# Performance work log

Hardware: AMD Instinct MI355X
Metric: run time of the kernel (lower is better)

Reference implementation:

```python
import jax, jax.numpy as jnp
import numpy as np

H = 1024
NH = 16
HD = H // NH  # 64

def setup_inputs() -> dict:
    key = jax.random.key(0)
    ks = jax.random.split(key, 6)
    B, S = 2, 2048
    hidden_states = jax.random.normal(ks[0], (B, S, H), dtype=jnp.float32)
    attention_mask = jnp.ones((B, S), dtype=jnp.int32)
    sc = 1.0 / np.sqrt(H)
    Wq = jax.random.normal(ks[1], (H, H), dtype=jnp.float32) * sc
    Wk = jax.random.normal(ks[2], (H, H), dtype=jnp.float32) * sc
    Wv = jax.random.normal(ks[3], (H, H), dtype=jnp.float32) * sc
    Wo = jax.random.normal(ks[4], (H, H), dtype=jnp.float32) * sc
    return {"hidden_states": hidden_states, "attention_mask": attention_mask,
            "Wq": Wq, "Wk": Wk, "Wv": Wv, "Wo": Wo}

def reference(hidden_states, attention_mask, Wq, Wk, Wv, Wo):
    B, S, _ = hidden_states.shape
    # nn.Linear(bias=False): y = x @ W.T
    q = hidden_states @ Wq.T
    k = hidden_states @ Wk.T
    v = hidden_states @ Wv.T
    # [B, NH, S, HD]
    q = q.reshape(B, S, NH, HD).transpose(0, 2, 1, 3)
    k = k.reshape(B, S, NH, HD).transpose(0, 2, 1, 3)
    v = v.reshape(B, S, NH, HD).transpose(0, 2, 1, 3)
    # ELU+1 feature map
    q = jax.nn.elu(q) + 1.0
    k = jax.nn.elu(k) + 1.0
    # [B, NH, S, S]
    attn = jnp.einsum('bhqd,bhkd->bhqk', q, k)
    mask = attention_mask[:, None, None, :]  # [B,1,1,S]
    attn = jnp.where(mask == 0, -jnp.inf, attn)
    attn = jax.nn.softmax(attn, axis=-1)
    # dropout p=0.0 (eval) -> identity
    out = jnp.einsum('bhqk,bhkd->bhqd', attn, v)
    out = out.transpose(0, 2, 1, 3).reshape(B, S, H)
    return out @ Wo.T
```

## Files before the change

### kernel.cpp

```cpp
#include <hip/hip_runtime.h>

#define H_ 1024
#define NH_ 16
#define HD_ 64
#define B_ 2
#define S_ 2048
#define BS_ 4096

typedef _Float16 half8 __attribute__((ext_vector_type(8)));
typedef _Float16 half4_t __attribute__((ext_vector_type(4)));
typedef float floatx4 __attribute__((ext_vector_type(4)));

#define LOG2E 1.44269504088896f

__device__ __forceinline__ void async_copy16(void* lds, const void* g) {
  __builtin_amdgcn_global_load_lds(
      (const __attribute__((address_space(1))) unsigned int*)g,
      (__attribute__((address_space(3))) unsigned int*)lds, 16, 0, 0);
}

__global__ __launch_bounds__(256) void cvt_all(
    const float* __restrict__ hs, const float* __restrict__ wq,
    const float* __restrict__ wk, const float* __restrict__ wv,
    const float* __restrict__ wo,
    _Float16* __restrict__ hs_h, _Float16* __restrict__ w_h) {
  int i = blockIdx.x * 256 + threadIdx.x;
  int idx = i * 4;
  const float* src; _Float16* dst; int off;
  if (idx < BS_ * H_) {
    src = hs; dst = hs_h; off = idx;
  } else {
    int j = idx - BS_ * H_;
    int w = j >> 20;
    off = j & ((1 << 20) - 1);
    src = (w == 0) ? wq : (w == 1) ? wk : (w == 2) ? wv : wo;
    dst = w_h + (size_t)w * (H_ * H_);
  }
  float4 f = *(const float4*)(src + off);
  half4_t o;
  o.x = (_Float16)f.x; o.y = (_Float16)f.y;
  o.z = (_Float16)f.z; o.w = (_Float16)f.w;
  *(half4_t*)(dst + off) = o;
}

__global__ __launch_bounds__(256) void qkv_gemm(
    const _Float16* __restrict__ A, const _Float16* __restrict__ Wall,
    _Float16* __restrict__ qh, _Float16* __restrict__ kh,
    _Float16* __restrict__ vt) {
  const int z = blockIdx.z;
  const _Float16* W = Wall + (size_t)z * (H_ * H_);
  const int rbase = blockIdx.y * 128;
  const int cbase = blockIdx.x * 128;
  __shared__ _Float16 As[128 * 32];
  __shared__ _Float16 Bs[128 * 32];
  const int tid = threadIdx.x, lane = tid & 63, w = tid >> 6;
  const int quad = lane >> 4, l16 = lane & 15;
  const int wr = (w >> 1) * 64, wc = (w & 1) * 64;

  floatx4 zero = {0.f, 0.f, 0.f, 0.f};
  floatx4 acc[4][4];
#pragma unroll
  for (int i = 0; i < 4; ++i)
#pragma unroll
    for (int j = 0; j < 4; ++j) acc[i][j] = zero;

  const int srow = w * 32 + (lane >> 2);
  const int sseg = (lane & 3) * 8;
  const _Float16* Ag = A + (size_t)(rbase + srow) * H_ + sseg;
  const _Float16* Bg = W + (size_t)(cbase + srow) * H_ + sseg;

  for (int k0 = 0; k0 < H_; k0 += 32) {
    async_copy16(&As[(w * 32) * 32], Ag + k0);
    async_copy16(&As[(w * 32 + 16) * 32], Ag + 16 * H_ + k0);
    async_copy16(&Bs[(w * 32) * 32], Bg + k0);
    async_copy16(&Bs[(w * 32 + 16) * 32], Bg + 16 * H_ + k0);
    __syncthreads();
    half8 af[4], bf[4];
#pragma unroll
    for (int t = 0; t < 4; ++t)
      af[t] = *(half8*)&As[(wr + t * 16 + l16) * 32 + quad * 8];
#pragma unroll
    for (int t = 0; t < 4; ++t)
      bf[t] = *(half8*)&Bs[(wc + t * 16 + l16) * 32 + quad * 8];
#pragma unroll
    for (int i = 0; i < 4; ++i)
#pragma unroll
      for (int j = 0; j < 4; ++j)
        acc[i][j] = __builtin_amdgcn_mfma_f32_16x16x32_f16(af[i], bf[j],
                                                           acc[i][j], 0, 0, 0);
    __syncthreads();
  }
#pragma unroll
  for (int i = 0; i < 4; ++i) {
    int r0 = rbase + wr + i * 16 + quad * 4;
    int b = r0 >> 11, sl0 = r0 & (S_ - 1);
#pragma unroll
    for (int j = 0; j < 4; ++j) {
      int col = cbase + wc + j * 16 + l16;
      int h = col >> 6, d = col & 63;
      if (z == 2) {
        half4_t pk;
#pragma unroll
        for (int r = 0; r < 4; ++r) pk[r] = (_Float16)acc[i][j][r];
        *(half4_t*)&vt[((size_t)(b * NH_ + h) * HD_ + d) * S_ + sl0] = pk;
      } else {
        _Float16* outp = (z == 0) ? qh : kh;
        float scale = (z == 0) ? LOG2E : 1.0f;
#pragma unroll
        for (int r = 0; r < 4; ++r) {
          float x = acc[i][j][r];
          x = ((x > 0.f) ? (x + 1.f) : __expf(x)) * scale;
          outp[((size_t)(b * NH_ + h) * S_ + sl0 + r) * HD_ + d] = (_Float16)x;
        }
      }
    }
  }
}

__global__ __launch_bounds__(256, 2) void flash_attn(
    const _Float16* __restrict__ qh, const _Float16* __restrict__ kh,
    const _Float16* __restrict__ vt, const int* __restrict__ mask,
    _Float16* __restrict__ attn_out) {
  const int bh = blockIdx.y, b = bh >> 4, h = bh & 15;
  const int qbase = blockIdx.x * 128;
  const int tid = threadIdx.x, w = tid >> 6, lane = tid & 63;
  const int quad = lane >> 4, l16 = lane & 15;

  __shared__ _Float16 Kt[2][128 * 64];
  __shared__ _Float16 Vt[2][64 * 128];

  const _Float16* Q = qh + (size_t)bh * (S_ * HD_);
  const _Float16* K = kh + (size_t)bh * (S_ * HD_);
  const _Float16* Vg = vt + (size_t)bh * (HD_ * S_);
  const int* Mb = mask + b * S_;

  half8 qf[2][2];
#pragma unroll
  for (int g = 0; g < 2; ++g) {
    int qr = qbase + w * 32 + g * 16 + l16;
    qf[g][0] = *(const half8*)&Q[qr * 64 + quad * 8];
    qf[g][1] = *(const half8*)&Q[qr * 64 + 32 + quad * 8];
  }

  floatx4 zero = {0.f, 0.f, 0.f, 0.f};
  floatx4 o[2][4];
#pragma unroll
  for (int g = 0; g < 2; ++g)
#pragma unroll
    for (int i = 0; i < 4; ++i) o[g][i] = zero;
  float mi[2] = {-3e38f, -3e38f}, li[2] = {0.f, 0.f};

  const int krow_off = lane >> 3;
  const int kslot = lane & 7;
  const int kchunk = kslot ^ (krow_off & 7);
  const int vrow_off = lane >> 4;
  const int vslot = lane & 15;

  {
#pragma unroll
    for (int u = 0; u < 4; ++u) {
      int kl = w * 32 + u * 8;
      async_copy16(&Kt[0][kl * 64], K + (size_t)(kl + krow_off) * 64 + kchunk * 8);
    }
#pragma unroll
    for (int u = 0; u < 4; ++u) {
      int d0 = w * 16 + u * 4 + vrow_off;
      int c0 = vslot ^ (d0 & 15);
      async_copy16(&Vt[0][(w * 16 + u * 4) * 128], Vg + (size_t)d0 * S_ + c0 * 8);
    }
  }

  for (int kt = 0; kt < S_ / 128; ++kt) {
    const int key0 = kt * 128;
    const int buf = kt & 1;
    __syncthreads();
    if (kt < S_ / 128 - 1) {
      const int key1 = key0 + 128;
#pragma unroll
      for (int u = 0; u < 4; ++u) {
        int kl = w * 32 + u * 8;
        async_copy16(&Kt[buf ^ 1][kl * 64],
                     K + (size_t)(key1 + kl + krow_off) * 64 + kchunk * 8);
      }
#pragma unroll
      for (int u = 0; u < 4; ++u) {
        int d0 = w * 16 + u * 4 + vrow_off;
        int c0 = vslot ^ (d0 & 15);
        async_copy16(&Vt[buf ^ 1][(w * 16 + u * 4) * 128],
                     Vg + (size_t)d0 * S_ + key1 + c0 * 8);
      }
    }
    int m0 = Mb[key0 + lane];
    int m1 = Mb[key0 + 64 + lane];

    const _Float16* Kb = &Kt[buf][0];
    const _Float16* Vb = &Vt[buf][0];

    floatx4 sa[2][8];
#pragma unroll
    for (int g = 0; g < 2; ++g)
#pragma unroll
      for (int ct = 0; ct < 8; ++ct) sa[g][ct] = zero;
    {
      int s0 = quad ^ (l16 & 7);
      int s1 = (4 + quad) ^ (l16 & 7);
#pragma unroll
      for (int ct = 0; ct < 8; ++ct) {
        int key = ct * 16 + l16;
        half8 bf0 = *(half8*)&Kb[key * 64 + s0 * 8];
        half8 bf1 = *(half8*)&Kb[key * 64 + s1 * 8];
        sa[0][ct] = __builtin_amdgcn_mfma_f32_16x16x32_f16(bf0, qf[0][0], sa[0][ct], 0, 0, 0);
        sa[0][ct] = __builtin_amdgcn_mfma_f32_16x16x32_f16(bf1, qf[0][1], sa[0][ct], 0, 0, 0);
        sa[1][ct] = __builtin_amdgcn_mfma_f32_16x16x32_f16(bf0, qf[1][0], sa[1][ct], 0, 0, 0);
        sa[1][ct] = __builtin_amdgcn_mfma_f32_16x16x32_f16(bf1, qf[1][1], sa[1][ct], 0, 0, 0);
      }
    }
    if (__any((m0 == 0) || (m1 == 0))) {
#pragma unroll
      for (int ct = 0; ct < 8; ++ct)
#pragma unroll
        for (int r = 0; r < 4; ++r)
          if (Mb[key0 + ct * 16 + quad * 4 + r] == 0) {
            sa[0][ct][r] = -1e30f;
            sa[1][ct][r] = -1e30f;
          }
    }
#pragma unroll
    for (int g = 0; g < 2; ++g) {
      float mx = sa[g][0][0];
#pragma unroll
      for (int ct = 0; ct < 8; ++ct)
#pragma unroll
        for (int r = 0; r < 4; ++r) mx = fmaxf(mx, sa[g][ct][r]);
      mx = fmaxf(mx, __shfl_xor(mx, 16));
      mx = fmaxf(mx, __shfl_xor(mx, 32));
      float mn = fmaxf(mi[g], mx);
      float alpha = __builtin_amdgcn_exp2f(mi[g] - mn);
      mi[g] = mn;
      float rs = 0.f;
#pragma unroll
      for (int ct = 0; ct < 8; ++ct)
#pragma unroll
        for (int r = 0; r < 4; ++r) {
          float p = __builtin_amdgcn_exp2f(sa[g][ct][r] - mn);
          sa[g][ct][r] = p;
          rs += p;
        }
      rs += __shfl_xor(rs, 16);
      rs += __shfl_xor(rs, 32);
      li[g] = li[g] * alpha + rs;
#pragma unroll
      for (int ct2 = 0; ct2 < 4; ++ct2) {
        o[g][ct2][0] *= alpha; o[g][ct2][1] *= alpha;
        o[g][ct2][2] *= alpha; o[g][ct2][3] *= alpha;
      }
    }
#pragma unroll
    for (int ct = 0; ct < 8; ++ct) {
      half4_t p0, p1;
#pragma unroll
      for (int r = 0; r < 4; ++r) {
        p0[r] = (_Float16)sa[0][ct][r];
        p1[r] = (_Float16)sa[1][ct][r];
      }
      int chunk = (2 * ct + (quad >> 1)) ^ l16;
      int off = chunk * 8 + (quad & 1) * 4;
#pragma unroll
      for (int ct2 = 0; ct2 < 4; ++ct2) {
        int d = ct2 * 16 + l16;
        half4_t vf = *(half4_t*)&Vb[d * 128 + off];
        o[0][ct2] = __builtin_amdgcn_mfma_f32_16x16x16f16(vf, p0, o[0][ct2], 0, 0, 0);
        o[1][ct2] = __builtin_amdgcn_mfma_f32_16x16x16f16(vf, p1, o[1][ct2], 0, 0, 0);
      }
    }
  }
#pragma unroll
  for (int g = 0; g < 2; ++g) {
    float inv = 1.0f / li[g];
    int row = qbase + w * 32 + g * 16 + l16;
#pragma unroll
    for (int ct2 = 0; ct2 < 4; ++ct2) {
      half4_t pk;
#pragma unroll
      for (int r = 0; r < 4; ++r) pk[r] = (_Float16)(o[g][ct2][r] * inv);
      int d = ct2 * 16 + quad * 4;
      *(half4_t*)&attn_out[((size_t)(b * S_ + row)) * H_ + h * HD_ + d] = pk;
    }
  }
}

__global__ __launch_bounds__(256) void out_gemm(
    const _Float16* __restrict__ A, const _Float16* __restrict__ W,
    float* __restrict__ out) {
  const int rbase = blockIdx.y * 128;
  const int cbase = blockIdx.x * 64;
  __shared__ _Float16 As[128 * 32];
  __shared__ _Float16 Bs[64 * 32];
  const int tid = threadIdx.x, lane = tid & 63, w = tid >> 6;
  const int quad = lane >> 4, l16 = lane & 15;

  floatx4 zero = {0.f, 0.f, 0.f, 0.f};
  floatx4 acc[2][4];
#pragma unroll
  for (int i = 0; i < 2; ++i)
#pragma unroll
    for (int j = 0; j < 4; ++j) acc[i][j] = zero;

  const int srowA = w * 32 + (lane >> 2);
  const int srowB = w * 16 + (lane >> 2);
  const int sseg = (lane & 3) * 8;
  const _Float16* Ag = A + (size_t)(rbase + srowA) * H_ + sseg;
  const _Float16* Bg = W + (size_t)(cbase + srowB) * H_ + sseg;

  for (int k0 = 0; k0 < H_; k0 += 32) {
    async_copy16(&As[(w * 32) * 32], Ag + k0);
    async_copy16(&As[(w * 32 + 16) * 32], Ag + 16 * H_ + k0);
    async_copy16(&Bs[(w * 16) * 32], Bg + k0);
    __syncthreads();
    half8 af[2], bf[4];
#pragma unroll
    for (int t = 0; t < 2; ++t)
      af[t] = *(half8*)&As[(w * 32 + t * 16 + l16) * 32 + quad * 8];
#pragma unroll
    for (int t = 0; t < 4; ++t)
      bf[t] = *(half8*)&Bs[(t * 16 + l16) * 32 + quad * 8];
#pragma unroll
    for (int i = 0; i < 2; ++i)
#pragma unroll
      for (int j = 0; j < 4; ++j)
        acc[i][j] = __builtin_amdgcn_mfma_f32_16x16x32_f16(af[i], bf[j],
                                                           acc[i][j], 0, 0, 0);
    __syncthreads();
  }
#pragma unroll
  for (int i = 0; i < 2; ++i) {
    int r0 = rbase + w * 32 + i * 16 + quad * 4;
#pragma unroll
    for (int j = 0; j < 4; ++j) {
      int col = cbase + j * 16 + l16;
#pragma unroll
      for (int r = 0; r < 4; ++r)
        out[(size_t)(r0 + r) * H_ + col] = acc[i][j][r];
    }
  }
}

extern "C" void kernel_launch(void* const* d_in, const int* in_sizes, int n_in,
                              void* d_out, int out_size, void* d_ws,
                              size_t ws_size, hipStream_t stream) {
  const float* hs = (const float*)d_in[0];
  const int* mask = (const int*)d_in[1];
  const float* Wq = (const float*)d_in[2];
  const float* Wk = (const float*)d_in[3];
  const float* Wv = (const float*)d_in[4];
  const float* Wo = (const float*)d_in[5];
  float* out = (float*)d_out;

  _Float16* p = (_Float16*)d_ws;
  _Float16* hs_h = p; p += (size_t)BS_ * H_;
  _Float16* w_h = p;  p += (size_t)4 * H_ * H_;
  _Float16* q_h = p;  p += (size_t)BS_ * H_;
  _Float16* k_h = p;  p += (size_t)BS_ * H_;
  _Float16* v_t = p;  p += (size_t)BS_ * H_;
  _Float16* ao_h = p; p += (size_t)BS_ * H_;

  cvt_all<<<8192, 256, 0, stream>>>(hs, Wq, Wk, Wv, Wo, hs_h, w_h);
  qkv_gemm<<<dim3(8, 32, 3), 256, 0, stream>>>(hs_h, w_h, q_h, k_h, v_t);
  flash_attn<<<dim3(16, 32), 256, 0, stream>>>(q_h, k_h, v_t, mask, ao_h);
  out_gemm<<<dim3(16, 32), 256, 0, stream>>>(ao_h, w_h + (size_t)3 * H_ * H_, out);
}
```

Measured before the change: 193.1 us.

## Use 8 waves of 16 query rows each in flash attention and skip redundant rescale

The attention kernel moves from 256 threads, where each wave handles 32 query rows, to 512 threads, where each wave handles 16 rows. Each wave then holds half the accumulator and score registers, which is meant to raise occupancy and hide latency. The wider block loads the shared K/V tiles cooperatively, with fewer copies per thread. The output rescale is skipped when no row maximum grows, and the max and sum reductions are split into independent chains. In exchange, each K fragment read from LDS is reused by only one query group instead of two, so LDS traffic per MFMA doubles.

```diff
diff --git a/kernel.cpp b/kernel.cpp
--- a/kernel.cpp
+++ b/kernel.cpp
@@ -117,7 +117,7 @@
   }
 }
 
-__global__ __launch_bounds__(256, 2) void flash_attn(
+__global__ __launch_bounds__(512, 4) void flash_attn(
     const _Float16* __restrict__ qh, const _Float16* __restrict__ kh,
     const _Float16* __restrict__ vt, const int* __restrict__ mask,
     _Float16* __restrict__ attn_out) {
@@ -134,21 +134,15 @@
   const _Float16* Vg = vt + (size_t)bh * (HD_ * S_);
   const int* Mb = mask + b * S_;
 
-  half8 qf[2][2];
-#pragma unroll
-  for (int g = 0; g < 2; ++g) {
-    int qr = qbase + w * 32 + g * 16 + l16;
-    qf[g][0] = *(const half8*)&Q[qr * 64 + quad * 8];
-    qf[g][1] = *(const half8*)&Q[qr * 64 + 32 + quad * 8];
-  }
+  const int qr = qbase + w * 16 + l16;
+  half8 qf0 = *(const half8*)&Q[qr * 64 + quad * 8];
+  half8 qf1 = *(const half8*)&Q[qr * 64 + 32 + quad * 8];
 
   floatx4 zero = {0.f, 0.f, 0.f, 0.f};
-  floatx4 o[2][4];
-#pragma unroll
-  for (int g = 0; g < 2; ++g)
-#pragma unroll
-    for (int i = 0; i < 4; ++i) o[g][i] = zero;
-  float mi[2] = {-3e38f, -3e38f}, li[2] = {0.f, 0.f};
+  floatx4 o[4];
+#pragma unroll
+  for (int i = 0; i < 4; ++i) o[i] = zero;
+  float mi = -3e38f, li = 0.f;
 
   const int krow_off = lane >> 3;
   const int kslot = lane & 7;
@@ -158,17 +152,20 @@
 
   {
 #pragma unroll
-    for (int u = 0; u < 4; ++u) {
-      int kl = w * 32 + u * 8;
+    for (int u = 0; u < 2; ++u) {
+      int kl = w * 16 + u * 8;
       async_copy16(&Kt[0][kl * 64], K + (size_t)(kl + krow_off) * 64 + kchunk * 8);
     }
 #pragma unroll
-    for (int u = 0; u < 4; ++u) {
-      int d0 = w * 16 + u * 4 + vrow_off;
+    for (int u = 0; u < 2; ++u) {
+      int d0 = w * 8 + u * 4 + vrow_off;
       int c0 = vslot ^ (d0 & 15);
-      async_copy16(&Vt[0][(w * 16 + u * 4) * 128], Vg + (size_t)d0 * S_ + c0 * 8);
-    }
-  }
+      async_copy16(&Vt[0][(w * 8 + u * 4) * 128], Vg + (size_t)d0 * S_ + c0 * 8);
+    }
+  }
+
+  const int s0 = quad ^ (l16 & 7);
+  const int s1 = (4 + quad) ^ (l16 & 7);
 
   for (int kt = 0; kt < S_ / 128; ++kt) {
     const int key0 = kt * 128;
@@ -177,16 +174,16 @@
     if (kt < S_ / 128 - 1) {
       const int key1 = key0 + 128;
 #pragma unroll
-      for (int u = 0; u < 4; ++u) {
-        int kl = w * 32 + u * 8;
+      for (int u = 0; u < 2; ++u) {
+        int kl = w * 16 + u * 8;
         async_copy16(&Kt[buf ^ 1][kl * 64],
                      K + (size_t)(key1 + kl + krow_off) * 64 + kchunk * 8);
       }
 #pragma unroll
-      for (int u = 0; u < 4; ++u) {
-        int d0 = w * 16 + u * 4 + vrow_off;
+      for (int u = 0; u < 2; ++u) {
+        int d0 = w * 8 + u * 4 + vrow_off;
         int c0 = vslot ^ (d0 & 15);
-        async_copy16(&Vt[buf ^ 1][(w * 16 + u * 4) * 128],
+        async_copy16(&Vt[buf ^ 1][(w * 8 + u * 4) * 128],
                      Vg + (size_t)d0 * S_ + key1 + c0 * 8);
       }
     }
@@ -196,93 +193,80 @@
     const _Float16* Kb = &Kt[buf][0];
     const _Float16* Vb = &Vt[buf][0];
 
-    floatx4 sa[2][8];
-#pragma unroll
-    for (int g = 0; g < 2; ++g)
-#pragma unroll
-      for (int ct = 0; ct < 8; ++ct) sa[g][ct] = zero;
-    {
-      int s0 = quad ^ (l16 & 7);
-      int s1 = (4 + quad) ^ (l16 & 7);
-#pragma unroll
-      for (int ct = 0; ct < 8; ++ct) {
-        int key = ct * 16 + l16;
-        half8 bf0 = *(half8*)&Kb[key * 64 + s0 * 8];
-        half8 bf1 = *(half8*)&Kb[key * 64 + s1 * 8];
-        sa[0][ct] = __builtin_amdgcn_mfma_f32_16x16x32_f16(bf0, qf[0][0], sa[0][ct], 0, 0, 0);
-        sa[0][ct] = __builtin_amdgcn_mfma_f32_16x16x32_f16(bf1, qf[0][1], sa[0][ct], 0, 0, 0);
-        sa[1][ct] = __builtin_amdgcn_mfma_f32_16x16x32_f16(bf0, qf[1][0], sa[1][ct], 0, 0, 0);
-        sa[1][ct] = __builtin_amdgcn_mfma_f32_16x16x32_f16(bf1, qf[1][1], sa[1][ct], 0, 0, 0);
-      }
+    floatx4 sa[8];
+#pragma unroll
+    for (int ct = 0; ct < 8; ++ct) sa[ct] = zero;
+#pragma unroll
+    for (int ct = 0; ct < 8; ++ct) {
+      int key = ct * 16 + l16;
+      half8 bf0 = *(half8*)&Kb[key * 64 + s0 * 8];
+      half8 bf1 = *(half8*)&Kb[key * 64 + s1 * 8];
+      sa[ct] = __builtin_amdgcn_mfma_f32_16x16x32_f16(bf0, qf0, sa[ct], 0, 0, 0);
+      sa[ct] = __builtin_amdgcn_mfma_f32_16x16x32_f16(bf1, qf1, sa[ct], 0, 0, 0);
     }
     if (__any((m0 == 0) || (m1 == 0))) {
 #pragma unroll
       for (int ct = 0; ct < 8; ++ct)
 #pragma unroll
         for (int r = 0; r < 4; ++r)
-          if (Mb[key0 + ct * 16 + quad * 4 + r] == 0) {
-            sa[0][ct][r] = -1e30f;
-            sa[1][ct][r] = -1e30f;
-          }
-    }
-#pragma unroll
-    for (int g = 0; g < 2; ++g) {
-      float mx = sa[g][0][0];
-#pragma unroll
-      for (int ct = 0; ct < 8; ++ct)
-#pragma unroll
-        for (int r = 0; r < 4; ++r) mx = fmaxf(mx, sa[g][ct][r]);
-      mx = fmaxf(mx, __shfl_xor(mx, 16));
-      mx = fmaxf(mx, __shfl_xor(mx, 32));
-      float mn = fmaxf(mi[g], mx);
-      float alpha = __builtin_amdgcn_exp2f(mi[g] - mn);
-      mi[g] = mn;
-      float rs = 0.f;
-#pragma unroll
-      for (int ct = 0; ct < 8; ++ct)
-#pragma unroll
-        for (int r = 0; r < 4; ++r) {
-          float p = __builtin_amdgcn_exp2f(sa[g][ct][r] - mn);
-          sa[g][ct][r] = p;
-          rs += p;
-        }
-      rs += __shfl_xor(rs, 16);
-      rs += __shfl_xor(rs, 32);
-      li[g] = li[g] * alpha + rs;
+          if (Mb[key0 + ct * 16 + quad * 4 + r] == 0) sa[ct][r] = -1e30f;
+    }
+    float t[8];
+#pragma unroll
+    for (int ct = 0; ct < 8; ++ct)
+      t[ct] = fmaxf(fmaxf(sa[ct][0], sa[ct][1]), fmaxf(sa[ct][2], sa[ct][3]));
+    float mx = fmaxf(fmaxf(fmaxf(t[0], t[1]), fmaxf(t[2], t[3])),
+                     fmaxf(fmaxf(t[4], t[5]), fmaxf(t[6], t[7])));
+    mx = fmaxf(mx, __shfl_xor(mx, 16));
+    mx = fmaxf(mx, __shfl_xor(mx, 32));
+    float mn = fmaxf(mi, mx);
+    float r0 = 0.f, r1 = 0.f, r2 = 0.f, r3 = 0.f;
+#pragma unroll
+    for (int ct = 0; ct < 8; ++ct) {
+      float p0 = __builtin_amdgcn_exp2f(sa[ct][0] - mn);
+      float p1 = __builtin_amdgcn_exp2f(sa[ct][1] - mn);
+      float p2 = __builtin_amdgcn_exp2f(sa[ct][2] - mn);
+      float p3 = __builtin_amdgcn_exp2f(sa[ct][3] - mn);
+      sa[ct][0] = p0; sa[ct][1] = p1; sa[ct][2] = p2; sa[ct][3] = p3;
+      r0 += p0; r1 += p1; r2 += p2; r3 += p3;
+    }
+    float rs = (r0 + r1) + (r2 + r3);
+    rs += __shfl_xor(rs, 16);
+    rs += __shfl_xor(rs, 32);
+    if (!__all(mx <= mi)) {
+      float alpha = __builtin_amdgcn_exp2f(mi - mn);
+      mi = mn;
+      li *= alpha;
 #pragma unroll
       for (int ct2 = 0; ct2 < 4; ++ct2) {
-        o[g][ct2][0] *= alpha; o[g][ct2][1] *= alpha;
-        o[g][ct2][2] *= alpha; o[g][ct2][3] *= alpha;
-      }
-    }
+        o[ct2][0] *= alpha; o[ct2][1] *= alpha;
+        o[ct2][2] *= alpha; o[ct2][3] *= alpha;
+      }
+    }
+    li += rs;
 #pragma unroll
     for (int ct = 0; ct < 8; ++ct) {
-      half4_t p0, p1;
-#pragma unroll
-      for (int r = 0; r < 4; ++r) {
-        p0[r] = (_Float16)sa[0][ct][r];
-        p1[r] = (_Float16)sa[1][ct][r];
-      }
+      half4_t p;
+#pragma unroll
+      for (int r = 0; r < 4; ++r) p[r] = (_Float16)sa[ct][r];
       int chunk = (2 * ct + (quad >> 1)) ^ l16;
       int off = chunk * 8 + (quad & 1) * 4;
 #pragma unroll
       for (int ct2 = 0; ct2 < 4; ++ct2) {
         int d = ct2 * 16 + l16;
         half4_t vf = *(half4_t*)&Vb[d * 128 + off];
-        o[0][ct2] = __builtin_amdgcn_mfma_f32_16x16x16f16(vf, p0, o[0][ct2], 0, 0, 0);
-        o[1][ct2] = __builtin_amdgcn_mfma_f32_16x16x16f16(vf, p1, o[1][ct2], 0, 0, 0);
-      }
-    }
-  }
-#pragma unroll
-  for (int g = 0; g < 2; ++g) {
-    float inv = 1.0f / li[g];
-    int row = qbase + w * 32 + g * 16 + l16;
+        o[ct2] = __builtin_amdgcn_mfma_f32_16x16x16f16(vf, p, o[ct2], 0, 0, 0);
+      }
+    }
+  }
+  {
+    float inv = 1.0f / li;
+    int row = qbase + w * 16 + l16;
 #pragma unroll
     for (int ct2 = 0; ct2 < 4; ++ct2) {
       half4_t pk;
 #pragma unroll
-      for (int r = 0; r < 4; ++r) pk[r] = (_Float16)(o[g][ct2][r] * inv);
+      for (int r = 0; r < 4; ++r) pk[r] = (_Float16)(o[ct2][r] * inv);
       int d = ct2 * 16 + quad * 4;
       *(half4_t*)&attn_out[((size_t)(b * S_ + row)) * H_ + h * HD_ + d] = pk;
     }
@@ -366,6 +350,6 @@
 
   cvt_all<<<8192, 256, 0, stream>>>(hs, Wq, Wk, Wv, Wo, hs_h, w_h);
   qkv_gemm<<<dim3(8, 32, 3), 256, 0, stream>>>(hs_h, w_h, q_h, k_h, v_t);
-  flash_attn<<<dim3(16, 32), 256, 0, stream>>>(q_h, k_h, v_t, mask, ao_h);
+  flash_attn<<<dim3(16, 32), 512, 0, stream>>>(q_h, k_h, v_t, mask, ao_h);
   out_gemm<<<dim3(16, 32), 256, 0, stream>>>(ao_h, w_h + (size_t)3 * H_ * H_, out);
 }
```

After: 199.0 us. 3.0% more time.

## Rewrite QKV GEMM with 256x256 tiles, 4-stage async pipeline and swizzled LDS

Applied to the files above, without the earlier changes.

Replaces the 128x128 QKV projection GEMM with a 512-thread 256x256 tile kernel that treats Q/K/V weights as one 3072-wide matrix. It uses a 4-deep async global-to-LDS pipeline with explicit vmcnt waits and one barrier per k-step, plus an XOR swizzle on LDS slots to avoid bank conflicts. It also raises MFMA priority and uses packed fp16 conversion for the V store. This aims to cut load stalls and barrier overhead, at the cost of 128KB of LDS and much higher register pressure. It also drops to 192 blocks, which could leave CUs underused.

```diff
diff --git a/kernel.cpp b/kernel.cpp
--- a/kernel.cpp
+++ b/kernel.cpp
@@ -9,6 +9,8 @@
 
 typedef _Float16 half8 __attribute__((ext_vector_type(8)));
 typedef _Float16 half4_t __attribute__((ext_vector_type(4)));
+typedef __fp16 fp16x2 __attribute__((ext_vector_type(2)));
+typedef __fp16 fp16x4 __attribute__((ext_vector_type(4)));
 typedef float floatx4 __attribute__((ext_vector_type(4)));
 
 #define LOG2E 1.44269504088896f
@@ -17,6 +19,13 @@
   __builtin_amdgcn_global_load_lds(
       (const __attribute__((address_space(1))) unsigned int*)g,
       (__attribute__((address_space(3))) unsigned int*)lds, 16, 0, 0);
+}
+
+__device__ __forceinline__ half4_t pack4(float a, float b, float c, float d) {
+  fp16x2 lo = __builtin_amdgcn_cvt_pkrtz(a, b);
+  fp16x2 hi = __builtin_amdgcn_cvt_pkrtz(c, d);
+  fp16x4 r = __builtin_shufflevector(lo, hi, 0, 1, 2, 3);
+  return __builtin_bit_cast(half4_t, r);
 }
 
 __global__ __launch_bounds__(256) void cvt_all(
@@ -43,72 +52,111 @@
   *(half4_t*)(dst + off) = o;
 }
 
-__global__ __launch_bounds__(256) void qkv_gemm(
+__global__ __launch_bounds__(512, 2) void qkv_fused(
     const _Float16* __restrict__ A, const _Float16* __restrict__ Wall,
     _Float16* __restrict__ qh, _Float16* __restrict__ kh,
     _Float16* __restrict__ vt) {
-  const int z = blockIdx.z;
-  const _Float16* W = Wall + (size_t)z * (H_ * H_);
-  const int rbase = blockIdx.y * 128;
-  const int cbase = blockIdx.x * 128;
-  __shared__ _Float16 As[128 * 32];
-  __shared__ _Float16 Bs[128 * 32];
+  const int rbase = blockIdx.y * 256;
+  const int cbase = blockIdx.x * 256;
+  const int z = cbase >> 10;
+  __shared__ _Float16 Ab[4][256 * 32];
+  __shared__ _Float16 Bb[4][256 * 32];
   const int tid = threadIdx.x, lane = tid & 63, w = tid >> 6;
   const int quad = lane >> 4, l16 = lane & 15;
-  const int wr = (w >> 1) * 64, wc = (w & 1) * 64;
+  const int wm = w >> 2, wn = w & 3;
 
   floatx4 zero = {0.f, 0.f, 0.f, 0.f};
-  floatx4 acc[4][4];
-#pragma unroll
-  for (int i = 0; i < 4; ++i)
-#pragma unroll
-    for (int j = 0; j < 4; ++j) acc[i][j] = zero;
-
-  const int srow = w * 32 + (lane >> 2);
-  const int sseg = (lane & 3) * 8;
-  const _Float16* Ag = A + (size_t)(rbase + srow) * H_ + sseg;
-  const _Float16* Bg = W + (size_t)(cbase + srow) * H_ + sseg;
-
-  for (int k0 = 0; k0 < H_; k0 += 32) {
-    async_copy16(&As[(w * 32) * 32], Ag + k0);
-    async_copy16(&As[(w * 32 + 16) * 32], Ag + 16 * H_ + k0);
-    async_copy16(&Bs[(w * 32) * 32], Bg + k0);
-    async_copy16(&Bs[(w * 32 + 16) * 32], Bg + 16 * H_ + k0);
-    __syncthreads();
-    half8 af[4], bf[4];
-#pragma unroll
-    for (int t = 0; t < 4; ++t)
-      af[t] = *(half8*)&As[(wr + t * 16 + l16) * 32 + quad * 8];
-#pragma unroll
-    for (int t = 0; t < 4; ++t)
-      bf[t] = *(half8*)&Bs[(wc + t * 16 + l16) * 32 + quad * 8];
-#pragma unroll
-    for (int i = 0; i < 4; ++i)
-#pragma unroll
-      for (int j = 0; j < 4; ++j)
-        acc[i][j] = __builtin_amdgcn_mfma_f32_16x16x32_f16(af[i], bf[j],
-                                                           acc[i][j], 0, 0, 0);
-    __syncthreads();
-  }
-#pragma unroll
-  for (int i = 0; i < 4; ++i) {
-    int r0 = rbase + wr + i * 16 + quad * 4;
+  floatx4 acc[8][4];
+#pragma unroll
+  for (int m = 0; m < 8; ++m)
+#pragma unroll
+    for (int n = 0; n < 4; ++n) acc[m][n] = zero;
+
+  const int srow = tid >> 2;
+  const int pslot = tid & 3;
+  const int sslot = pslot ^ ((tid >> 3) & 3);
+  const _Float16* Ag = A + (size_t)(rbase + srow) * H_ + sslot * 8;
+  const _Float16* Bg = Wall + (size_t)(cbase + srow) * H_ + sslot * 8;
+
+  auto STAGE = [&](int t) {
+    const int k0 = t * 32;
+    _Float16* ab = &Ab[t & 3][0];
+    _Float16* bb = &Bb[t & 3][0];
+#pragma unroll
+    for (int u = 0; u < 2; ++u)
+      async_copy16(ab + (size_t)(u * 128 + srow) * 32 + pslot * 8,
+                   Ag + (size_t)u * 128 * H_ + k0);
+#pragma unroll
+    for (int u = 0; u < 2; ++u)
+      async_copy16(bb + (size_t)(u * 128 + srow) * 32 + pslot * 8,
+                   Bg + (size_t)u * 128 * H_ + k0);
+  };
+
+  const int rsw = (l16 >> 1) & 3;
+  auto COMPUTE = [&](int t) {
+    const _Float16* Ap = &Ab[t & 3][0];
+    const _Float16* Bp = &Bb[t & 3][0];
+    half8 af[8], bf[4];
+#pragma unroll
+    for (int m = 0; m < 8; ++m) {
+      int row = wm * 128 + m * 16 + l16;
+      af[m] = *(const half8*)&Ap[row * 32 + ((quad ^ rsw) * 8)];
+    }
+#pragma unroll
+    for (int n = 0; n < 4; ++n) {
+      int row = wn * 64 + n * 16 + l16;
+      bf[n] = *(const half8*)&Bp[row * 32 + ((quad ^ rsw) * 8)];
+    }
+    __builtin_amdgcn_s_setprio(1);
+#pragma unroll
+    for (int m = 0; m < 8; ++m)
+#pragma unroll
+      for (int n = 0; n < 4; ++n)
+        acc[m][n] = __builtin_amdgcn_mfma_f32_16x16x32_f16(af[m], bf[n],
+                                                           acc[m][n], 0, 0, 0);
+    __builtin_amdgcn_s_setprio(0);
+  };
+
+  STAGE(0); STAGE(1); STAGE(2);
+
+  for (int t = 0; t < 30; ++t) {
+    asm volatile("s_waitcnt vmcnt(8)" ::: "memory");
+    __builtin_amdgcn_sched_barrier(0);
+    __builtin_amdgcn_s_barrier();
+    __builtin_amdgcn_sched_barrier(0);
+    if (t < 29) STAGE(t + 3);
+    COMPUTE(t);
+  }
+  asm volatile("s_waitcnt vmcnt(4)" ::: "memory");
+  __builtin_amdgcn_sched_barrier(0);
+  __builtin_amdgcn_s_barrier();
+  __builtin_amdgcn_sched_barrier(0);
+  COMPUTE(30);
+  asm volatile("s_waitcnt vmcnt(0)" ::: "memory");
+  __builtin_amdgcn_sched_barrier(0);
+  __builtin_amdgcn_s_barrier();
+  __builtin_amdgcn_sched_barrier(0);
+  COMPUTE(31);
+
+#pragma unroll
+  for (int m = 0; m < 8; ++m) {
+    int r0 = rbase + wm * 128 + m * 16 + quad * 4;
     int b = r0 >> 11, sl0 = r0 & (S_ - 1);
 #pragma unroll
-    for (int j = 0; j < 4; ++j) {
-      int col = cbase + wc + j * 16 + l16;
-      int h = col >> 6, d = col & 63;
+    for (int n = 0; n < 4; ++n) {
+      int col = cbase + wn * 64 + n * 16 + l16;
+      int c = col & 1023;
+      int h = c >> 6, d = c & 63;
       if (z == 2) {
-        half4_t pk;
-#pragma unroll
-        for (int r = 0; r < 4; ++r) pk[r] = (_Float16)acc[i][j][r];
+        half4_t pk = pack4(acc[m][n][0], acc[m][n][1], acc[m][n][2],
+                           acc[m][n][3]);
         *(half4_t*)&vt[((size_t)(b * NH_ + h) * HD_ + d) * S_ + sl0] = pk;
       } else {
         _Float16* outp = (z == 0) ? qh : kh;
         float scale = (z == 0) ? LOG2E : 1.0f;
 #pragma unroll
         for (int r = 0; r < 4; ++r) {
-          float x = acc[i][j][r];
+          float x = acc[m][n][r];
           x = ((x > 0.f) ? (x + 1.f) : __expf(x)) * scale;
           outp[((size_t)(b * NH_ + h) * S_ + sl0 + r) * HD_ + d] = (_Float16)x;
         }
@@ -365,7 +413,7 @@
   _Float16* ao_h = p; p += (size_t)BS_ * H_;
 
   cvt_all<<<8192, 256, 0, stream>>>(hs, Wq, Wk, Wv, Wo, hs_h, w_h);
-  qkv_gemm<<<dim3(8, 32, 3), 256, 0, stream>>>(hs_h, w_h, q_h, k_h, v_t);
+  qkv_fused<<<dim3(12, 16), 512, 0, stream>>>(hs_h, w_h, q_h, k_h, v_t);
   flash_attn<<<dim3(16, 32), 256, 0, stream>>>(q_h, k_h, v_t, mask, ao_h);
   out_gemm<<<dim3(16, 32), 256, 0, stream>>>(ao_h, w_h + (size_t)3 * H_ * H_, out);
 }
```

Measured after the change: 205.7 us. 1.07x slower.

## Software-pipeline PV matmul of previous tile with softmax of current tile

Applied to the files above, without the earlier changes.

Restructures the flash-attention key loop so the P·V MFMAs for tile kt-1 are interleaved with the max/exp softmax work for tile kt. P values are carried between iterations in register arrays, and V gets a third LDS buffer so the previous tile's V stays valid while the next one is prefetched. The aim is to hide the exp/reduction latency behind matrix-core work. In exchange it uses more LDS (80KB per block) and more registers, which could reduce occupancy or cause spills.

```diff
diff --git a/kernel.cpp b/kernel.cpp
--- a/kernel.cpp
+++ b/kernel.cpp
@@ -127,7 +127,7 @@
   const int quad = lane >> 4, l16 = lane & 15;
 
   __shared__ _Float16 Kt[2][128 * 64];
-  __shared__ _Float16 Vt[2][64 * 128];
+  __shared__ _Float16 Vt[3][64 * 128];
 
   const _Float16* Q = qh + (size_t)bh * (S_ * HD_);
   const _Float16* K = kh + (size_t)bh * (S_ * HD_);
@@ -170,50 +170,53 @@
     }
   }
 
-  for (int kt = 0; kt < S_ / 128; ++kt) {
+  const int s0 = quad ^ (l16 & 7);
+  const int s1 = (4 + quad) ^ (l16 & 7);
+
+  half4_t pA[2][8], pB[2][8];
+
+  auto TILE = [&](int kt, half4_t (&pin)[2][8], half4_t (&pout)[2][8],
+                  int vprev, int vnext, bool dopv) {
     const int key0 = kt * 128;
-    const int buf = kt & 1;
     __syncthreads();
     if (kt < S_ / 128 - 1) {
       const int key1 = key0 + 128;
+      _Float16* Kd = &Kt[(kt + 1) & 1][0];
+      _Float16* Vd = &Vt[vnext][0];
 #pragma unroll
       for (int u = 0; u < 4; ++u) {
         int kl = w * 32 + u * 8;
-        async_copy16(&Kt[buf ^ 1][kl * 64],
+        async_copy16(Kd + kl * 64,
                      K + (size_t)(key1 + kl + krow_off) * 64 + kchunk * 8);
       }
 #pragma unroll
       for (int u = 0; u < 4; ++u) {
         int d0 = w * 16 + u * 4 + vrow_off;
         int c0 = vslot ^ (d0 & 15);
-        async_copy16(&Vt[buf ^ 1][(w * 16 + u * 4) * 128],
+        async_copy16(Vd + (w * 16 + u * 4) * 128,
                      Vg + (size_t)d0 * S_ + key1 + c0 * 8);
       }
     }
     int m0 = Mb[key0 + lane];
     int m1 = Mb[key0 + 64 + lane];
 
-    const _Float16* Kb = &Kt[buf][0];
-    const _Float16* Vb = &Vt[buf][0];
-
-    floatx4 sa[2][8];
+    const _Float16* Kb = &Kt[kt & 1][0];
+    const _Float16* Vb = &Vt[vprev][0];
+
+    floatx4 sb[2][8];
 #pragma unroll
     for (int g = 0; g < 2; ++g)
 #pragma unroll
-      for (int ct = 0; ct < 8; ++ct) sa[g][ct] = zero;
-    {
-      int s0 = quad ^ (l16 & 7);
-      int s1 = (4 + quad) ^ (l16 & 7);
-#pragma unroll
-      for (int ct = 0; ct < 8; ++ct) {
-        int key = ct * 16 + l16;
-        half8 bf0 = *(half8*)&Kb[key * 64 + s0 * 8];
-        half8 bf1 = *(half8*)&Kb[key * 64 + s1 * 8];
-        sa[0][ct] = __builtin_amdgcn_mfma_f32_16x16x32_f16(bf0, qf[0][0], sa[0][ct], 0, 0, 0);
-        sa[0][ct] = __builtin_amdgcn_mfma_f32_16x16x32_f16(bf1, qf[0][1], sa[0][ct], 0, 0, 0);
-        sa[1][ct] = __builtin_amdgcn_mfma_f32_16x16x32_f16(bf0, qf[1][0], sa[1][ct], 0, 0, 0);
-        sa[1][ct] = __builtin_amdgcn_mfma_f32_16x16x32_f16(bf1, qf[1][1], sa[1][ct], 0, 0, 0);
-      }
+      for (int ct = 0; ct < 8; ++ct) sb[g][ct] = zero;
+#pragma unroll
+    for (int ct = 0; ct < 8; ++ct) {
+      int key = ct * 16 + l16;
+      half8 bf0 = *(half8*)&Kb[key * 64 + s0 * 8];
+      half8 bf1 = *(half8*)&Kb[key * 64 + s1 * 8];
+      sb[0][ct] = __builtin_amdgcn_mfma_f32_16x16x32_f16(bf0, qf[0][0], sb[0][ct], 0, 0, 0);
+      sb[0][ct] = __builtin_amdgcn_mfma_f32_16x16x32_f16(bf1, qf[0][1], sb[0][ct], 0, 0, 0);
+      sb[1][ct] = __builtin_amdgcn_mfma_f32_16x16x32_f16(bf0, qf[1][0], sb[1][ct], 0, 0, 0);
+      sb[1][ct] = __builtin_amdgcn_mfma_f32_16x16x32_f16(bf1, qf[1][1], sb[1][ct], 0, 0, 0);
     }
     if (__any((m0 == 0) || (m1 == 0))) {
 #pragma unroll
@@ -221,56 +224,111 @@
 #pragma unroll
         for (int r = 0; r < 4; ++r)
           if (Mb[key0 + ct * 16 + quad * 4 + r] == 0) {
-            sa[0][ct][r] = -1e30f;
-            sa[1][ct][r] = -1e30f;
+            sb[0][ct][r] = -1e30f;
+            sb[1][ct][r] = -1e30f;
           }
     }
+
+#define PVC(ct)                                                              \
+  if (dopv) {                                                                \
+    int chunk = (2 * (ct) + (quad >> 1)) ^ l16;                              \
+    int off = chunk * 8 + (quad & 1) * 4;                                    \
+    _Pragma("unroll") for (int ct2 = 0; ct2 < 4; ++ct2) {                    \
+      int d = ct2 * 16 + l16;                                                \
+      half4_t vf = *(half4_t*)&Vb[d * 128 + off];                            \
+      o[0][ct2] = __builtin_amdgcn_mfma_f32_16x16x16f16(vf, pin[0][ct],      \
+                                                        o[0][ct2], 0, 0, 0); \
+      o[1][ct2] = __builtin_amdgcn_mfma_f32_16x16x16f16(vf, pin[1][ct],      \
+                                                        o[1][ct2], 0, 0, 0); \
+    }                                                                        \
+  }
+
+    PVC(0); PVC(1);
+    float tt[2][8];
+#pragma unroll
+    for (int g = 0; g < 2; ++g)
+#pragma unroll
+      for (int ct = 0; ct < 8; ++ct)
+        tt[g][ct] = fmaxf(fmaxf(sb[g][ct][0], sb[g][ct][1]),
+                          fmaxf(sb[g][ct][2], sb[g][ct][3]));
+    PVC(2); PVC(3);
+    float mx[2], mn[2], alpha[2];
 #pragma unroll
     for (int g = 0; g < 2; ++g) {
-      float mx = sa[g][0][0];
-#pragma unroll
-      for (int ct = 0; ct < 8; ++ct)
-#pragma unroll
-        for (int r = 0; r < 4; ++r) mx = fmaxf(mx, sa[g][ct][r]);
-      mx = fmaxf(mx, __shfl_xor(mx, 16));
-      mx = fmaxf(mx, __shfl_xor(mx, 32));
-      float mn = fmaxf(mi[g], mx);
-      float alpha = __builtin_amdgcn_exp2f(mi[g] - mn);
-      mi[g] = mn;
-      float rs = 0.f;
-#pragma unroll
-      for (int ct = 0; ct < 8; ++ct)
-#pragma unroll
-        for (int r = 0; r < 4; ++r) {
-          float p = __builtin_amdgcn_exp2f(sa[g][ct][r] - mn);
-          sa[g][ct][r] = p;
-          rs += p;
-        }
-      rs += __shfl_xor(rs, 16);
-      rs += __shfl_xor(rs, 32);
-      li[g] = li[g] * alpha + rs;
+      float m = fmaxf(fmaxf(fmaxf(tt[g][0], tt[g][1]), fmaxf(tt[g][2], tt[g][3])),
+                      fmaxf(fmaxf(tt[g][4], tt[g][5]), fmaxf(tt[g][6], tt[g][7])));
+      m = fmaxf(m, __shfl_xor(m, 16));
+      mx[g] = fmaxf(m, __shfl_xor(m, 32));
+    }
+    PVC(4); PVC(5);
+#pragma unroll
+    for (int g = 0; g < 2; ++g) {
+      mn[g] = fmaxf(mi[g], mx[g]);
+      alpha[g] = __builtin_amdgcn_exp2f(mi[g] - mn[g]);
+    }
+    PVC(6); PVC(7);
+    float rs[2];
+#pragma unroll
+    for (int g = 0; g < 2; ++g) {
+      float r0 = 0.f, r1 = 0.f, r2 = 0.f, r3 = 0.f;
+#pragma unroll
+      for (int ct = 0; ct < 8; ++ct) {
+        float p0 = __builtin_amdgcn_exp2f(sb[g][ct][0] - mn[g]);
+        float p1 = __builtin_amdgcn_exp2f(sb[g][ct][1] - mn[g]);
+        float p2 = __builtin_amdgcn_exp2f(sb[g][ct][2] - mn[g]);
+        float p3 = __builtin_amdgcn_exp2f(sb[g][ct][3] - mn[g]);
+        sb[g][ct][0] = p0; sb[g][ct][1] = p1;
+        sb[g][ct][2] = p2; sb[g][ct][3] = p3;
+        r0 += p0; r1 += p1; r2 += p2; r3 += p3;
+      }
+      float s = (r0 + r1) + (r2 + r3);
+      s += __shfl_xor(s, 16);
+      rs[g] = s + __shfl_xor(s, 32);
+    }
+#undef PVC
+#pragma unroll
+    for (int g = 0; g < 2; ++g) {
+      mi[g] = mn[g];
+      li[g] = li[g] * alpha[g] + rs[g];
 #pragma unroll
       for (int ct2 = 0; ct2 < 4; ++ct2) {
-        o[g][ct2][0] *= alpha; o[g][ct2][1] *= alpha;
-        o[g][ct2][2] *= alpha; o[g][ct2][3] *= alpha;
-      }
-    }
+        o[g][ct2][0] *= alpha[g]; o[g][ct2][1] *= alpha[g];
+        o[g][ct2][2] *= alpha[g]; o[g][ct2][3] *= alpha[g];
+      }
+    }
+#pragma unroll
+    for (int g = 0; g < 2; ++g)
+#pragma unroll
+      for (int ct = 0; ct < 8; ++ct) {
+        half4_t pk;
+#pragma unroll
+        for (int r = 0; r < 4; ++r) pk[r] = (_Float16)sb[g][ct][r];
+        pout[g][ct] = pk;
+      }
+  };
+
+  int vcur = 0;
+  for (int k2 = 0; k2 < S_ / 128; k2 += 2) {
+    int vnext = (vcur == 2) ? 0 : vcur + 1;
+    int vprev = (vcur == 0) ? 2 : vcur - 1;
+    TILE(k2, pB, pA, vprev, vnext, k2 > 0);
+    int vcur1 = vnext;
+    int vnext1 = (vcur1 == 2) ? 0 : vcur1 + 1;
+    TILE(k2 + 1, pA, pB, vcur, vnext1, true);
+    vcur = vnext1;
+  }
+  {
+    const _Float16* Vb = &Vt[0][0];
 #pragma unroll
     for (int ct = 0; ct < 8; ++ct) {
-      half4_t p0, p1;
-#pragma unroll
-      for (int r = 0; r < 4; ++r) {
-        p0[r] = (_Float16)sa[0][ct][r];
-        p1[r] = (_Float16)sa[1][ct][r];
-      }
       int chunk = (2 * ct + (quad >> 1)) ^ l16;
       int off = chunk * 8 + (quad & 1) * 4;
 #pragma unroll
       for (int ct2 = 0; ct2 < 4; ++ct2) {
         int d = ct2 * 16 + l16;
         half4_t vf = *(half4_t*)&Vb[d * 128 + off];
-        o[0][ct2] = __builtin_amdgcn_mfma_f32_16x16x16f16(vf, p0, o[0][ct2], 0, 0, 0);
-        o[1][ct2] = __builtin_amdgcn_mfma_f32_16x16x16f16(vf, p1, o[1][ct2], 0, 0, 0);
+        o[0][ct2] = __builtin_amdgcn_mfma_f32_16x16x16f16(vf, pB[0][ct], o[0][ct2], 0, 0, 0);
+        o[1][ct2] = __builtin_amdgcn_mfma_f32_16x16x16f16(vf, pB[1][ct], o[1][ct2], 0, 0, 0);
       }
     }
   }
```

After: 198.4 us. 2.7% more time.
